# Optimization experiments

Hardware: AMD Instinct MI355X
Metric: run time of the kernel (lower is better)

Reference implementation:

```python
import jax, jax.numpy as jnp
import numpy as np

NTOKENS = 102400
NHID = 128
NTOK_PER_CLASS = 320
NCLASSES = int(np.ceil(NTOKENS / NTOK_PER_CLASS))  # 320
NTOKENS_ACTUAL = NCLASSES * NTOK_PER_CLASS          # 102400
BATCH = 1024


def setup_inputs() -> dict:
    key = jax.random.key(0)
    k1, k2, k3 = jax.random.split(key, 3)
    initrange = 0.1
    return {
        "inputs": jax.random.normal(k1, (BATCH, NHID), dtype=jnp.float32),
        "layer_top_W": jax.random.uniform(k2, (NHID, NCLASSES), dtype=jnp.float32, minval=-initrange, maxval=initrange),
        "layer_top_b": jnp.zeros((NCLASSES,), dtype=jnp.float32),
        "layer_bottom_W": jax.random.uniform(k3, (NTOK_PER_CLASS, NHID), dtype=jnp.float32, minval=-initrange, maxval=initrange),
        "layer_bottom_b": jnp.zeros((NCLASSES,), dtype=jnp.float32),
    }


def reference(inputs, layer_top_W, layer_top_b, layer_bottom_W, layer_bottom_b):
    # labels = arange(ntokens_actual); pos_top = labels // per_class; pos_bottom = labels % per_class
    # The original gathers layer_bottom_W[pos_bottom] ([ntokens_actual, nhid]) before a full matmul;
    # mathematically this is the small matmul inputs @ bottom_W.T tiled nclasses times along dim 1.
    batch = inputs.shape[0]
    pos_bottom_base = jnp.arange(NTOK_PER_CLASS)  # bottom-index pattern within one class block

    layer_top_logits = inputs @ layer_top_W + layer_top_b            # [B, nclasses]
    bottom_block = inputs @ layer_bottom_W.T + layer_bottom_b[pos_bottom_base]  # [B, per_class]

    # repeat_interleave(top, per_class, dim=1) + tile(bottom, nclasses) fused via broadcast:
    target_logits = (layer_top_logits[:, :, None] + bottom_block[:, None, :]).reshape(
        batch, NTOKENS_ACTUAL
    )  # [B, ntokens_actual]
    return target_logits
```

## Files before the change

### kernel.cpp

```cpp
#include <hip/hip_runtime.h>


#define BATCH      1024
#define NHID       128
#define NCLASSES   320
#define PER_CLASS  320
#define ROW_ELEMS  (NCLASSES * PER_CLASS)
#define ROW_F4     (ROW_ELEMS / 4)
#define PC_F4      (PER_CLASS / 4)
#define LPR        (NCLASSES + PER_CLASS)
#define LPR_F4     (LPR / 4)
#define WS_BYTES   ((size_t)BATCH * LPR * sizeof(float))

#define STHREADS   256
#define SGRID      2048
#define TOTAL_F4   (BATCH * ROW_F4)
#define SSTRIDE    (SGRID * STHREADS)
#define SITERS     (TOTAL_F4 / SSTRIDE)

typedef float f32x4 __attribute__((ext_vector_type(4)));

__global__ __launch_bounds__(LPR) void hs_logits_kernel(
    const float* __restrict__ inputs,
    const float* __restrict__ top_W,
    const float* __restrict__ top_b,
    const float* __restrict__ bottom_W,
    const float* __restrict__ bottom_b,
    float* __restrict__ ws)
{
    __shared__ __align__(16) float s_in[NHID];
    const int b   = blockIdx.x;
    const int tid = threadIdx.x;

    if (tid < NHID) s_in[tid] = inputs[b * NHID + tid];
    __syncthreads();

    float acc;
    if (tid < NCLASSES) {
        acc = top_b[tid];
        #pragma unroll 8
        for (int k = 0; k < NHID; ++k)
            acc += s_in[k] * top_W[k * NCLASSES + tid];
    } else {
        const int t = tid - NCLASSES;
        acc = bottom_b[t];
        const f32x4* w4 = (const f32x4*)(bottom_W + t * NHID);
        #pragma unroll 8
        for (int k4 = 0; k4 < NHID / 4; ++k4) {
            f32x4 w = w4[k4];
            acc += s_in[4*k4+0]*w.x + s_in[4*k4+1]*w.y
                 + s_in[4*k4+2]*w.z + s_in[4*k4+3]*w.w;
        }
    }
    ws[b * LPR + tid] = acc;
}

__global__ __launch_bounds__(STHREADS, 8) void hs_stream_kernel(
    const float* __restrict__ ws,
    float* __restrict__ out)
{
    const f32x4* __restrict__ ws4  = (const f32x4*)ws;
    f32x4* __restrict__ out4 = (f32x4*)out;

    unsigned g = blockIdx.x * STHREADS + threadIdx.x;
    #pragma unroll 5
    for (int it = 0; it < SITERS; ++it, g += SSTRIDE) {
        const unsigned b  = g / ROW_F4;
        const unsigned r  = g - b * ROW_F4;
        const unsigned c  = r / PC_F4;
        const unsigned t4 = r - c * PC_F4;
        const float tv = ws[b * LPR + c];
        const f32x4 bv = ws4[b * LPR_F4 + (NCLASSES/4) + t4];
        f32x4 v;
        v.x = tv + bv.x;
        v.y = tv + bv.y;
        v.z = tv + bv.z;
        v.w = tv + bv.w;
        __builtin_nontemporal_store(v, &out4[g]);
    }
}

#define HALVES      2
#define CLS_PER_BLK (NCLASSES / HALVES)
#define FTHREADS    320
#define C_PER_ITER  (FTHREADS / PC_F4)
#define NITER       (CLS_PER_BLK / C_PER_ITER)

__global__ __launch_bounds__(FTHREADS) void hs_fused_kernel(
    const float* __restrict__ inputs, const float* __restrict__ top_W,
    const float* __restrict__ top_b, const float* __restrict__ bottom_W,
    const float* __restrict__ bottom_b, float* __restrict__ out)
{
    __shared__ __align__(16) float s_in[NHID];
    __shared__ float s_top[CLS_PER_BLK];
    __shared__ __align__(16) float s_bot[PER_CLASS];
    const int b = blockIdx.x, h = blockIdx.y, tid = threadIdx.x;
    if (tid < NHID) s_in[tid] = inputs[b * NHID + tid];
    __syncthreads();
    for (int j = tid; j < CLS_PER_BLK + PER_CLASS; j += FTHREADS) {
        float acc;
        if (j < CLS_PER_BLK) {
            const int c = h * CLS_PER_BLK + j;
            acc = top_b[c];
            #pragma unroll 8
            for (int k = 0; k < NHID; ++k) acc += s_in[k] * top_W[k * NCLASSES + c];
            s_top[j] = acc;
        } else {
            const int t = j - CLS_PER_BLK;
            acc = bottom_b[t];
            const f32x4* w4 = (const f32x4*)(bottom_W + t * NHID);
            #pragma unroll 8
            for (int k4 = 0; k4 < NHID / 4; ++k4) {
                f32x4 w = w4[k4];
                acc += s_in[4*k4+0]*w.x + s_in[4*k4+1]*w.y + s_in[4*k4+2]*w.z + s_in[4*k4+3]*w.w;
            }
            s_bot[t] = acc;
        }
    }
    __syncthreads();
    const int c_off = tid / PC_F4;
    const int t4    = tid - c_off * PC_F4;
    const f32x4 bv  = ((const f32x4*)s_bot)[t4];
    f32x4* outp = (f32x4*)out + (size_t)b * ROW_F4 + h * (CLS_PER_BLK * PC_F4) + c_off * PC_F4 + t4;
    #pragma unroll 8
    for (int it = 0; it < NITER; ++it) {
        const float tv = s_top[it * C_PER_ITER + c_off];
        f32x4 v;
        v.x = tv + bv.x; v.y = tv + bv.y; v.z = tv + bv.z; v.w = tv + bv.w;
        outp[it * (C_PER_ITER * PC_F4)] = v;
    }
}

extern "C" void kernel_launch(void* const* d_in, const int* in_sizes, int n_in,
                              void* d_out, int out_size, void* d_ws, size_t ws_size,
                              hipStream_t stream) {
    const float* inputs   = (const float*)d_in[0];
    const float* top_W    = (const float*)d_in[1];
    const float* top_b    = (const float*)d_in[2];
    const float* bottom_W = (const float*)d_in[3];
    const float* bottom_b = (const float*)d_in[4];
    float* out = (float*)d_out;

    if (d_ws != nullptr && ws_size >= WS_BYTES) {
        float* ws = (float*)d_ws;
        hs_logits_kernel<<<BATCH, LPR, 0, stream>>>(inputs, top_W, top_b, bottom_W, bottom_b, ws);
        hs_stream_kernel<<<SGRID, STHREADS, 0, stream>>>(ws, out);
    } else {
        hs_fused_kernel<<<dim3(BATCH, HALVES), FTHREADS, 0, stream>>>(
            inputs, top_W, top_b, bottom_W, bottom_b, out);
    }
}
```

Measured before the change: 463.1 us.

## Stage per-row logits in LDS and assign one wavefront per output row

The streaming kernel now runs 256 blocks. Each block copies four rows of top and bottom logits from workspace into shared memory, then each wavefront writes one full output row. This replaces the grid-stride loop, which reread the workspace from global or L2 and did a 32-bit division per element. The store also switches from nontemporal to a normal store. With only 256 blocks there may be too few waves in flight to saturate write bandwidth, and the store cache behaviour changes.

```diff
diff --git a/kernel.cpp b/kernel.cpp
--- a/kernel.cpp
+++ b/kernel.cpp
@@ -12,11 +12,10 @@
 #define LPR_F4     (LPR / 4)
 #define WS_BYTES   ((size_t)BATCH * LPR * sizeof(float))
 
-#define STHREADS   256
-#define SGRID      2048
-#define TOTAL_F4   (BATCH * ROW_F4)
-#define SSTRIDE    (SGRID * STHREADS)
-#define SITERS     (TOTAL_F4 / SSTRIDE)
+#define K2_BLOCKS  256
+#define K2_THREADS 256
+#define RPB        (BATCH / K2_BLOCKS)
+#define ITERS_PW   (ROW_F4 / 64)
 
 typedef float f32x4 __attribute__((ext_vector_type(4)));
 
@@ -55,28 +54,40 @@
     ws[b * LPR + tid] = acc;
 }
 
-__global__ __launch_bounds__(STHREADS, 8) void hs_stream_kernel(
+__global__ __launch_bounds__(K2_THREADS) void hs_stream_kernel(
     const float* __restrict__ ws,
     float* __restrict__ out)
 {
-    const f32x4* __restrict__ ws4  = (const f32x4*)ws;
-    f32x4* __restrict__ out4 = (f32x4*)out;
+    __shared__ __align__(16) float s_log[RPB][LPR];
 
-    unsigned g = blockIdx.x * STHREADS + threadIdx.x;
-    #pragma unroll 5
-    for (int it = 0; it < SITERS; ++it, g += SSTRIDE) {
-        const unsigned b  = g / ROW_F4;
-        const unsigned r  = g - b * ROW_F4;
-        const unsigned c  = r / PC_F4;
-        const unsigned t4 = r - c * PC_F4;
-        const float tv = ws[b * LPR + c];
-        const f32x4 bv = ws4[b * LPR_F4 + (NCLASSES/4) + t4];
+    const int b   = blockIdx.x;
+    const int tid = threadIdx.x;
+
+    const f32x4* wsrc = (const f32x4*)(ws + (size_t)b * RPB * LPR);
+    f32x4* sdst = (f32x4*)&s_log[0][0];
+    for (int j = tid; j < RPB * LPR_F4; j += K2_THREADS)
+        sdst[j] = wsrc[j];
+    __syncthreads();
+
+    const int w    = tid >> 6;
+    const int lane = tid & 63;
+    const float* srow  = s_log[w];
+    const f32x4* srow4 = (const f32x4*)(srow + NCLASSES);
+    f32x4* outp = (f32x4*)out + (size_t)(b * RPB + w) * ROW_F4;
+
+    #pragma unroll 8
+    for (int it = 0; it < ITERS_PW; ++it) {
+        const unsigned g  = lane + it * 64;
+        const unsigned c  = g / PC_F4;
+        const unsigned t4 = g - c * PC_F4;
+        const float tv = srow[c];
+        const f32x4 bv = srow4[t4];
         f32x4 v;
         v.x = tv + bv.x;
         v.y = tv + bv.y;
         v.z = tv + bv.z;
         v.w = tv + bv.w;
-        __builtin_nontemporal_store(v, &out4[g]);
+        outp[g] = v;
     }
 }
 
@@ -144,7 +155,7 @@
     if (d_ws != nullptr && ws_size >= WS_BYTES) {
         float* ws = (float*)d_ws;
         hs_logits_kernel<<<BATCH, LPR, 0, stream>>>(inputs, top_W, top_b, bottom_W, bottom_b, ws);
-        hs_stream_kernel<<<SGRID, STHREADS, 0, stream>>>(ws, out);
+        hs_stream_kernel<<<K2_BLOCKS, K2_THREADS, 0, stream>>>(ws, out);
     } else {
         hs_fused_kernel<<<dim3(BATCH, HALVES), FTHREADS, 0, stream>>>(
             inputs, top_W, top_b, bottom_W, bottom_b, out);
```

Measured after the change: 450.0 us. 2.8% less time.
